# Kernel optimization log

Measured on AMD Instinct MI355X. Metric: run time of the kernel, lower is better.

The kernel has to match this reference:

```python
import jax, jax.numpy as jnp
import numpy as np

NEIGHBORS = 16  # init kwarg 'neighbors'


def _mlp(x, params):
    # SetTransform with reduction='none': pointwise MLP, ReLU between layers, linear output
    for W, b in params[:-1]:
        x = jax.nn.relu(x @ W + b)
    W, b = params[-1]
    return x @ W + b


def setup_inputs() -> dict:
    key = jax.random.key(0)
    B, K, P, DIM, C_IN = 4, 2048, 4096, 3, 64
    C_MID, C_OUT = 32, 128
    WH = 32          # weight_hidden sizes
    FH = 256         # final_hidden size
    FIN = C_IN * C_MID  # 2048, final_conv input

    ks = jax.random.split(key, 16)

    def lin(k, fan_in, fan_out):
        k1, k2 = jax.random.split(k)
        s = 1.0 / np.sqrt(fan_in)
        W = jax.random.uniform(k1, (fan_in, fan_out), minval=-s, maxval=s, dtype=jnp.float32)
        b = jax.random.uniform(k2, (fan_out,), minval=-s, maxval=s, dtype=jnp.float32)
        return W, b

    wc0_W, wc0_b = lin(ks[0], DIM, WH)
    wc1_W, wc1_b = lin(ks[1], WH, WH)
    wc2_W, wc2_b = lin(ks[2], WH, C_MID)
    fc0_W, fc0_b = lin(ks[3], FIN, FH)
    fc1_W, fc1_b = lin(ks[4], FH, C_OUT)

    return {
        "keys": jax.random.normal(ks[5], (B, K, DIM), dtype=jnp.float32),
        "points": jax.random.normal(ks[6], (B, P, DIM), dtype=jnp.float32),
        "feats": jax.random.normal(ks[7], (B, P, C_IN), dtype=jnp.float32),
        "wc0_W": wc0_W, "wc0_b": wc0_b,
        "wc1_W": wc1_W, "wc1_b": wc1_b,
        "wc2_W": wc2_W, "wc2_b": wc2_b,
        "fc0_W": fc0_W, "fc0_b": fc0_b,
        "fc1_W": fc1_W, "fc1_b": fc1_b,
    }


def reference(keys, points, feats,
              wc0_W, wc0_b, wc1_W, wc1_b, wc2_W, wc2_b,
              fc0_W, fc0_b, fc1_W, fc1_b):
    B, K, _ = keys.shape
    # Euclidean dist_fn: rel_pos [B,K,P,dim], squared dist [B,K,P]; all points valid
    dist_vec = points[:, None, :, :] - keys[:, :, None, :]
    dist = jnp.sum(dist_vec * dist_vec, axis=-1)
    # k smallest distances -> neighbor indices [B,K,N]
    _, idxs = jax.lax.top_k(-dist, NEIGHBORS)
    # gather relative positions [B,K,N,dim] and neighbor features [B,K,N,c_in]
    neighbor_rel = jnp.take_along_axis(dist_vec, idxs[..., None], axis=2)
    b_idx = jnp.arange(B)[:, None, None]
    neighbor_feats = feats[b_idx, idxs]
    # per-edge weight MLP: [B,K,N,dim] -> [B,K,N,c_mid]
    m = _mlp(neighbor_rel, [(wc0_W, wc0_b), (wc1_W, wc1_b), (wc2_W, wc2_b)])
    # masked matmul aggregation (all neighbors valid under euclidean dist_fn):
    # m^T @ neighbor_feats -> [B,K,c_mid,c_in], flattened to [B,K,c_mid*c_in]
    e = jnp.einsum('bknm,bknc->bkmc', m, neighbor_feats).reshape(B, K, -1)
    # final pointwise MLP -> [B,K,c_out]
    return _mlp(e, [(fc0_W, fc0_b), (fc1_W, fc1_b)])
```

## Files before the change

kernel.cpp:

```cpp
#include <hip/hip_runtime.h>
#include <cfloat>
#include <climits>

#define BATCH 4
#define KQ    2048
#define NP    4096
#define CIN   64
#define CMID  32
#define NB    16
#define NBINS 4096
#define CANDCAP 256
#define QPB   8

typedef short   bf16x8  __attribute__((ext_vector_type(8)));
typedef float   floatx4 __attribute__((ext_vector_type(4)));

__device__ __forceinline__ unsigned short f2bf(float f) {
  unsigned u = __float_as_uint(f);
  u = (u + 0x7fffu + ((u >> 16) & 1u)) >> 16;
  return (unsigned short)u;
}

__device__ __forceinline__ void load_lds16(const void* g, void* l) {
  __builtin_amdgcn_global_load_lds(
      (const __attribute__((address_space(1))) unsigned int*)g,
      (__attribute__((address_space(3))) unsigned int*)l, 16, 0, 0);
}

__global__ __launch_bounds__(256) void select_topk(
    const float* __restrict__ keys, const float* __restrict__ points,
    int* __restrict__ nidx_g) {
  __shared__ int   hist[NBINS];
  __shared__ int   psum[256];
  __shared__ float cand_d[CANDCAP];
  __shared__ int   cand_i[CANDCAP];
  __shared__ int   nidx[NB];
  __shared__ int   sel_cnt, cand_cnt, sBin, sCbelow;

  const int tid = threadIdx.x;
  const int b   = blockIdx.x >> 11;

  for (int i = tid; i < NBINS; i += 256) hist[i] = 0;
  if (tid == 0) { sel_cnt = 0; cand_cnt = 0; }

  const float kx = keys[blockIdx.x * 3 + 0];
  const float ky = keys[blockIdx.x * 3 + 1];
  const float kz = keys[blockIdx.x * 3 + 2];
  __syncthreads();

  const float4* pv =
      reinterpret_cast<const float4*>(points + (size_t)b * NP * 3) + (size_t)tid * 12;
  float f[48];
#pragma unroll
  for (int c = 0; c < 12; ++c) {
    const float4 v = pv[c];
    f[c * 4 + 0] = v.x; f[c * 4 + 1] = v.y; f[c * 4 + 2] = v.z; f[c * 4 + 3] = v.w;
  }
  float dreg[16];
#pragma unroll
  for (int j = 0; j < 16; ++j) {
    const float dx = f[j * 3 + 0] - kx;
    const float dy = f[j * 3 + 1] - ky;
    const float dz = f[j * 3 + 2] - kz;
    const float d  = dx * dx + dy * dy + dz * dz;
    dreg[j] = d;
    atomicAdd(&hist[__float_as_uint(d) >> 19], 1);
  }
  __syncthreads();

  {
    const int base = tid * 16;
    int s = 0;
#pragma unroll
    for (int j = 0; j < 16; ++j) s += hist[base + j];
    psum[tid] = s;
  }
  __syncthreads();

  if (tid < 64) {
    const int q = psum[tid * 4] + psum[tid * 4 + 1] + psum[tid * 4 + 2] + psum[tid * 4 + 3];
    int incl = q;
#pragma unroll
    for (int off = 1; off < 64; off <<= 1) {
      int u = __shfl_up(incl, off);
      if (tid >= off) incl += u;
    }
    unsigned long long bal = __ballot(incl >= NB);
    int firstlane = __ffsll((long long)bal) - 1;
    if (tid == firstlane) {
      int cum = incl - q;
      int bin = -1;
      for (int t = 0; t < 4 && bin < 0; ++t) {
        const int ps = psum[tid * 4 + t];
        if (cum + ps >= NB) {
          const int b0 = (tid * 4 + t) * 16;
          for (int j = 0; j < 16; ++j) {
            const int h = hist[b0 + j];
            if (cum + h >= NB) { bin = b0 + j; break; }
            cum += h;
          }
        } else cum += ps;
      }
      sBin = bin; sCbelow = cum;
    }
  }
  __syncthreads();

  const unsigned B = (unsigned)sBin;
#pragma unroll
  for (int j = 0; j < 16; ++j) {
    const int i = tid * 16 + j;
    const unsigned bk = __float_as_uint(dreg[j]) >> 19;
    if (bk < B) {
      int pos = atomicAdd(&sel_cnt, 1);
      nidx[pos] = i;
    } else if (bk == B) {
      int pos = atomicAdd(&cand_cnt, 1);
      if (pos < CANDCAP) { cand_d[pos] = dreg[j]; cand_i[pos] = i; }
    }
  }
  __syncthreads();

  if (tid < 64) {
    const int rem = NB - sCbelow;
    const int cc  = min(cand_cnt, CANDCAP);
    for (int s = 0; s < rem; ++s) {
      float bd = FLT_MAX; int bi = INT_MAX; int bp = -1;
      for (int j = tid; j < cc; j += 64) {
        float d = cand_d[j]; int ii = cand_i[j];
        if (d < bd || (d == bd && ii < bi)) { bd = d; bi = ii; bp = j; }
      }
#pragma unroll
      for (int off = 32; off > 0; off >>= 1) {
        float od = __shfl_down(bd, off);
        int   oi = __shfl_down(bi, off);
        int   op = __shfl_down(bp, off);
        if (od < bd || (od == bd && oi < bi)) { bd = od; bi = oi; bp = op; }
      }
      if (tid == 0) { nidx[sCbelow + s] = bi; cand_d[bp] = FLT_MAX; }
    }
  }
  __syncthreads();

  if (tid < NB) nidx_g[blockIdx.x * NB + tid] = nidx[tid];
}

__global__ __launch_bounds__(256) void edge_mlp_e(
    const float* __restrict__ keys, const float* __restrict__ points,
    const float* __restrict__ feats, const int* __restrict__ nidx_g,
    const float* __restrict__ wc0_W, const float* __restrict__ wc0_b,
    const float* __restrict__ wc1_W, const float* __restrict__ wc1_b,
    const float* __restrict__ wc2_W, const float* __restrict__ wc2_b,
    unsigned short* __restrict__ E) {
  __shared__ float w0[96], b0v[32], w1[1024], b1v[32], w2[1024], b2v[32];
  __shared__ int   idx_s[QPB * NB];
  __shared__ float m_all[QPB * NB][CMID + 1];
  __shared__ __align__(16) float f_all[QPB * NB][CIN + 4];

  const int tid = threadIdx.x;
  const int q0  = blockIdx.x * QPB;
  const int b   = q0 >> 11;

  if (tid < 96) w0[tid] = wc0_W[tid];
  for (int i = tid; i < 1024; i += 256) { w1[i] = wc1_W[i]; w2[i] = wc2_W[i]; }
  if (tid < 32) { b0v[tid] = wc0_b[tid]; b1v[tid] = wc1_b[tid]; b2v[tid] = wc2_b[tid]; }
  if (tid < QPB * NB) idx_s[tid] = nidx_g[q0 * NB + tid];
  __syncthreads();

  if (tid < QPB * NB) {
    const int q   = tid >> 4;
    const int idx = idx_s[tid];
    const float* p  = points + ((size_t)b * NP + idx) * 3;
    const float* kq = keys + (size_t)(q0 + q) * 3;
    const float rx = p[0] - kq[0], ry = p[1] - kq[1], rz = p[2] - kq[2];
    float h1[32], h2[32];
#pragma unroll
    for (int o = 0; o < 32; ++o)
      h1[o] = fmaxf(0.f, rx * w0[o] + ry * w0[32 + o] + rz * w0[64 + o] + b0v[o]);
#pragma unroll
    for (int o = 0; o < 32; ++o) {
      float a = b1v[o];
#pragma unroll
      for (int i = 0; i < 32; ++i) a += h1[i] * w1[i * 32 + o];
      h2[o] = fmaxf(0.f, a);
    }
#pragma unroll
    for (int o = 0; o < 32; ++o) {
      float a = b2v[o];
#pragma unroll
      for (int i = 0; i < 32; ++i) a += h2[i] * w2[i * 32 + o];
      m_all[tid][o] = a;
    }
  } else {
    const int u  = tid - 128;
    const int cq = u & 15;
    for (int p = (u >> 4); p < QPB * NB; p += 8) {
      const int idx = idx_s[p];
      const float4 v = *reinterpret_cast<const float4*>(
          feats + ((size_t)b * NP + idx) * CIN + cq * 4);
      *reinterpret_cast<float4*>(&f_all[p][cq * 4]) = v;
    }
  }
  __syncthreads();

  const int g  = tid >> 4;
  const int cq = tid & 15;
  for (int p = g; p < QPB * CMID; p += 16) {
    const int q = p >> 5, mid = p & 31;
    float4 a = {0.f, 0.f, 0.f, 0.f};
#pragma unroll
    for (int n = 0; n < NB; ++n) {
      const float mv = m_all[q * NB + n][mid];
      const float4 fv = *reinterpret_cast<const float4*>(&f_all[q * NB + n][cq * 4]);
      a.x += mv * fv.x; a.y += mv * fv.y; a.z += mv * fv.z; a.w += mv * fv.w;
    }
    ushort4 o;
    o.x = f2bf(a.x); o.y = f2bf(a.y); o.z = f2bf(a.z); o.w = f2bf(a.w);
    *reinterpret_cast<ushort4*>(&E[(size_t)(q0 + q) * 2048 + mid * 64 + cq * 4]) = o;
  }
}

__global__ __launch_bounds__(256) void transpose_bf16(
    const float* __restrict__ W, unsigned short* __restrict__ WT,
    int K, int N) {
  __shared__ float t[32][33];
  const int k0 = blockIdx.x * 32, n0 = blockIdx.y * 32;
  const int tx = threadIdx.x & 31, ty = threadIdx.x >> 5;
#pragma unroll
  for (int p = 0; p < 4; ++p)
    t[ty + p * 8][tx] = W[(size_t)(k0 + ty + p * 8) * N + n0 + tx];
  __syncthreads();
#pragma unroll
  for (int p = 0; p < 4; ++p)
    WT[(size_t)(n0 + ty + p * 8) * K + k0 + tx] = f2bf(t[tx][ty + p * 8]);
}

template <int KDIM, bool RELU, bool OUTBF16>
__global__ __launch_bounds__(256) void gemm_mfma(
    const unsigned short* __restrict__ A,
    const unsigned short* __restrict__ Bt,
    const float* __restrict__ bias,
    void* __restrict__ Cout, int ldc) {
  __shared__ __align__(16) unsigned short Al[64 * 128];
  __shared__ __align__(16) unsigned short Bl[64 * 128];
  const int tid  = threadIdx.x;
  const int m0   = blockIdx.x * 64, n0 = blockIdx.y * 64;
  const int wv   = tid >> 6, lane = tid & 63;
  const int quad = lane >> 4, s = lane & 15;
  const int moff = (wv & 1) * 32, noff = (wv >> 1) * 32;
  const int lr   = lane >> 4;
  const int lc   = lane & 15;

  floatx4 acc[2][2] = {{{0.f,0.f,0.f,0.f},{0.f,0.f,0.f,0.f}},
                       {{0.f,0.f,0.f,0.f},{0.f,0.f,0.f,0.f}}};

  for (int k0 = 0; k0 < KDIM; k0 += 128) {
#pragma unroll
    for (int t = 0; t < 4; ++t) {
      const int R0 = wv * 16 + t * 4;
      const int r  = R0 + lr;
      const int gc = lc ^ (r & 7);
      load_lds16(A  + (size_t)(m0 + r) * KDIM + k0 + gc * 8, &Al[R0 * 128]);
      load_lds16(Bt + (size_t)(n0 + r) * KDIM + k0 + gc * 8, &Bl[R0 * 128]);
    }
    __syncthreads();
#pragma unroll
    for (int h = 0; h < 4; ++h) {
      bf16x8 af[2], bfr[2];
#pragma unroll
      for (int i = 0; i < 2; ++i) {
        const int r = moff + i * 16 + s;
        af[i] = *reinterpret_cast<const bf16x8*>(
            &Al[(size_t)r * 128 + ((((h << 2) | quad) ^ (r & 7)) << 3)]);
      }
#pragma unroll
      for (int j = 0; j < 2; ++j) {
        const int r = noff + j * 16 + s;
        bfr[j] = *reinterpret_cast<const bf16x8*>(
            &Bl[(size_t)r * 128 + ((((h << 2) | quad) ^ (r & 7)) << 3)]);
      }
#pragma unroll
      for (int i = 0; i < 2; ++i)
#pragma unroll
        for (int j = 0; j < 2; ++j)
          acc[i][j] = __builtin_amdgcn_mfma_f32_16x16x32_bf16(af[i], bfr[j], acc[i][j], 0, 0, 0);
    }
    __syncthreads();
  }

#pragma unroll
  for (int i = 0; i < 2; ++i)
#pragma unroll
    for (int j = 0; j < 2; ++j) {
      const int col = n0 + noff + j * 16 + s;
      const float bv = bias[col];
#pragma unroll
      for (int r = 0; r < 4; ++r) {
        const int row = m0 + moff + i * 16 + quad * 4 + r;
        float v = acc[i][j][r] + bv;
        if (RELU) v = fmaxf(v, 0.f);
        if (OUTBF16)
          ((unsigned short*)Cout)[(size_t)row * ldc + col] = f2bf(v);
        else
          ((float*)Cout)[(size_t)row * ldc + col] = v;
      }
    }
}

extern "C" void kernel_launch(void* const* d_in, const int* in_sizes, int n_in,
                              void* d_out, int out_size, void* d_ws, size_t ws_size,
                              hipStream_t stream) {
  const float* keys   = (const float*)d_in[0];
  const float* points = (const float*)d_in[1];
  const float* feats  = (const float*)d_in[2];
  const float* wc0_W  = (const float*)d_in[3];
  const float* wc0_b  = (const float*)d_in[4];
  const float* wc1_W  = (const float*)d_in[5];
  const float* wc1_b  = (const float*)d_in[6];
  const float* wc2_W  = (const float*)d_in[7];
  const float* wc2_b  = (const float*)d_in[8];
  const float* fc0_W  = (const float*)d_in[9];
  const float* fc0_b  = (const float*)d_in[10];
  const float* fc1_W  = (const float*)d_in[11];
  const float* fc1_b  = (const float*)d_in[12];
  float* out = (float*)d_out;

  const int M = BATCH * KQ;
  char* ws = (char*)d_ws;
  unsigned short* E    = (unsigned short*)(ws);
  unsigned short* H16  = (unsigned short*)(ws + (size_t)33554432);
  unsigned short* W0T  = (unsigned short*)(ws + (size_t)37748736);
  unsigned short* W1T  = (unsigned short*)(ws + (size_t)38797312);
  int*            nidx = (int*)(ws + (size_t)38862848);

  select_topk<<<M, 256, 0, stream>>>(keys, points, nidx);
  transpose_bf16<<<dim3(64, 8), 256, 0, stream>>>(fc0_W, W0T, 2048, 256);
  transpose_bf16<<<dim3(8, 4), 256, 0, stream>>>(fc1_W, W1T, 256, 128);
  edge_mlp_e<<<M / QPB, 256, 0, stream>>>(keys, points, feats, nidx,
                                          wc0_W, wc0_b, wc1_W, wc1_b, wc2_W, wc2_b, E);
  gemm_mfma<2048, true,  true ><<<dim3(M / 64, 4), 256, 0, stream>>>(E, W0T, fc0_b, H16, 256);
  gemm_mfma<256,  false, false><<<dim3(M / 64, 2), 256, 0, stream>>>(H16, W1T, fc1_b, out, 128);
}
```

Measured before the change: 187.8 us.

## Split edge MLP across all threads and register-tile aggregation with bf16 LDS

The edge MLP now runs on all 256 threads instead of 128. Each half-block computes 16 of the 32 hidden and output units per edge, exchanging the second-layer activations through LDS. Neighbor features and edge weights are staged in LDS as bf16, and the m^T·f aggregation uses a 4x8 register tile per lane, with wider LDS reads and 16-byte E stores. This aims to remove the idle half-block during the MLP and cut LDS traffic in the aggregation. It adds two extra barriers and reduces the precision of m and feats before aggregation.

```diff
diff --git a/kernel.cpp b/kernel.cpp
--- a/kernel.cpp
+++ b/kernel.cpp
@@ -19,6 +19,9 @@
   unsigned u = __float_as_uint(f);
   u = (u + 0x7fffu + ((u >> 16) & 1u)) >> 16;
   return (unsigned short)u;
+}
+__device__ __forceinline__ float bf2f(unsigned short u) {
+  return __uint_as_float((unsigned)u << 16);
 }
 
 __device__ __forceinline__ void load_lds16(const void* g, void* l) {
@@ -154,8 +157,10 @@
     unsigned short* __restrict__ E) {
   __shared__ float w0[96], b0v[32], w1[1024], b1v[32], w2[1024], b2v[32];
   __shared__ int   idx_s[QPB * NB];
-  __shared__ float m_all[QPB * NB][CMID + 1];
-  __shared__ __align__(16) float f_all[QPB * NB][CIN + 4];
+  __shared__ __align__(16) unsigned short m_bf[QPB * NB][40];
+  __shared__ __align__(16) char u_mem[128 * 144];
+  float (*h2_all)[33]        = reinterpret_cast<float(*)[33]>(u_mem);
+  unsigned short (*f_bf)[72] = reinterpret_cast<unsigned short(*)[72]>(u_mem);
 
   const int tid = threadIdx.x;
   const int q0  = blockIdx.x * QPB;
@@ -167,56 +172,92 @@
   if (tid < QPB * NB) idx_s[tid] = nidx_g[q0 * NB + tid];
   __syncthreads();
 
-  if (tid < QPB * NB) {
-    const int q   = tid >> 4;
-    const int idx = idx_s[tid];
+  const int edge = tid & 127;
+  const int half = tid >> 7;
+  const int ob   = half * 16;
+  const int qe   = edge >> 4;
+  const int idx  = idx_s[edge];
+  {
     const float* p  = points + ((size_t)b * NP + idx) * 3;
-    const float* kq = keys + (size_t)(q0 + q) * 3;
+    const float* kq = keys + (size_t)(q0 + qe) * 3;
     const float rx = p[0] - kq[0], ry = p[1] - kq[1], rz = p[2] - kq[2];
-    float h1[32], h2[32];
+
+    float h1[32];
 #pragma unroll
     for (int o = 0; o < 32; ++o)
       h1[o] = fmaxf(0.f, rx * w0[o] + ry * w0[32 + o] + rz * w0[64 + o] + b0v[o]);
 #pragma unroll
-    for (int o = 0; o < 32; ++o) {
+    for (int j = 0; j < 16; ++j) {
+      const int o = ob + j;
       float a = b1v[o];
 #pragma unroll
       for (int i = 0; i < 32; ++i) a += h1[i] * w1[i * 32 + o];
-      h2[o] = fmaxf(0.f, a);
-    }
-#pragma unroll
-    for (int o = 0; o < 32; ++o) {
-      float a = b2v[o];
-#pragma unroll
-      for (int i = 0; i < 32; ++i) a += h2[i] * w2[i * 32 + o];
-      m_all[tid][o] = a;
-    }
-  } else {
-    const int u  = tid - 128;
-    const int cq = u & 15;
-    for (int p = (u >> 4); p < QPB * NB; p += 8) {
-      const int idx = idx_s[p];
-      const float4 v = *reinterpret_cast<const float4*>(
-          feats + ((size_t)b * NP + idx) * CIN + cq * 4);
-      *reinterpret_cast<float4*>(&f_all[p][cq * 4]) = v;
-    }
-  }
-  __syncthreads();
-
-  const int g  = tid >> 4;
-  const int cq = tid & 15;
-  for (int p = g; p < QPB * CMID; p += 16) {
-    const int q = p >> 5, mid = p & 31;
-    float4 a = {0.f, 0.f, 0.f, 0.f};
-#pragma unroll
-    for (int n = 0; n < NB; ++n) {
-      const float mv = m_all[q * NB + n][mid];
-      const float4 fv = *reinterpret_cast<const float4*>(&f_all[q * NB + n][cq * 4]);
-      a.x += mv * fv.x; a.y += mv * fv.y; a.z += mv * fv.z; a.w += mv * fv.w;
-    }
-    ushort4 o;
-    o.x = f2bf(a.x); o.y = f2bf(a.y); o.z = f2bf(a.z); o.w = f2bf(a.w);
-    *reinterpret_cast<ushort4*>(&E[(size_t)(q0 + q) * 2048 + mid * 64 + cq * 4]) = o;
+      h2_all[edge][o] = fmaxf(a, 0.f);
+    }
+  }
+  __syncthreads();
+
+  float mo[16];
+#pragma unroll
+  for (int j = 0; j < 16; ++j) {
+    const int o = ob + j;
+    float a = b2v[o];
+#pragma unroll
+    for (int i = 0; i < 32; ++i) a += h2_all[edge][i] * w2[i * 32 + o];
+    mo[j] = a;
+  }
+#pragma unroll
+  for (int j = 0; j < 8; ++j) {
+    const unsigned lo = f2bf(mo[2 * j]), hi = f2bf(mo[2 * j + 1]);
+    *reinterpret_cast<unsigned*>(&m_bf[edge][ob + 2 * j]) = lo | (hi << 16);
+  }
+  __syncthreads();
+
+#pragma unroll
+  for (int t = 0; t < 8; ++t) {
+    const int task = tid + t * 256;
+    const int row = task >> 4, ch = task & 15;
+    const float4 v = *reinterpret_cast<const float4*>(
+        feats + ((size_t)b * NP + idx_s[row]) * CIN + ch * 4);
+    ushort4 o4;
+    o4.x = f2bf(v.x); o4.y = f2bf(v.y); o4.z = f2bf(v.z); o4.w = f2bf(v.w);
+    *reinterpret_cast<ushort4*>(&f_bf[row][ch * 4]) = o4;
+  }
+  __syncthreads();
+
+  const int wv = tid >> 6, lane = tid & 63;
+  const int co = lane & 7, mg = lane >> 3;
+#pragma unroll
+  for (int it = 0; it < 2; ++it) {
+    const int q = wv + it * 4;
+    float acc[4][8] = {};
+#pragma unroll
+    for (int n = 0; n < 16; ++n) {
+      const int row = q * 16 + n;
+      const ushort4 m4 = *reinterpret_cast<const ushort4*>(&m_bf[row][mg * 4]);
+      const float mv[4] = {bf2f(m4.x), bf2f(m4.y), bf2f(m4.z), bf2f(m4.w)};
+      const uint4 fv = *reinterpret_cast<const uint4*>(&f_bf[row][co * 8]);
+      float fc[8];
+      fc[0] = __uint_as_float(fv.x << 16); fc[1] = __uint_as_float(fv.x & 0xffff0000u);
+      fc[2] = __uint_as_float(fv.y << 16); fc[3] = __uint_as_float(fv.y & 0xffff0000u);
+      fc[4] = __uint_as_float(fv.z << 16); fc[5] = __uint_as_float(fv.z & 0xffff0000u);
+      fc[6] = __uint_as_float(fv.w << 16); fc[7] = __uint_as_float(fv.w & 0xffff0000u);
+#pragma unroll
+      for (int i = 0; i < 4; ++i)
+#pragma unroll
+        for (int j = 0; j < 8; ++j) acc[i][j] += mv[i] * fc[j];
+    }
+    unsigned short* Eq = E + (size_t)(q0 + q) * 2048;
+#pragma unroll
+    for (int i = 0; i < 4; ++i) {
+      const int mid = mg * 4 + i;
+      uint4 o;
+      o.x = (unsigned)f2bf(acc[i][0]) | ((unsigned)f2bf(acc[i][1]) << 16);
+      o.y = (unsigned)f2bf(acc[i][2]) | ((unsigned)f2bf(acc[i][3]) << 16);
+      o.z = (unsigned)f2bf(acc[i][4]) | ((unsigned)f2bf(acc[i][5]) << 16);
+      o.w = (unsigned)f2bf(acc[i][6]) | ((unsigned)f2bf(acc[i][7]) << 16);
+      *reinterpret_cast<uint4*>(&Eq[mid * 64 + co * 8]) = o;
+    }
   }
 }
 
```

New measurement: 184.1 us. About the same (-1.9%).
